# Performance work log

Measured on AMD Instinct MI355X. Metric: run time of the kernel, lower is better.

The kernel has to match this reference:

```python
import jax, jax.numpy as jnp
import numpy as np
from jax import lax

K = 20
SLOPE = 0.01


def setup_inputs() -> dict:
    key = jax.random.key(0)
    k1, k2 = jax.random.split(key)
    x = jax.random.normal(k1, (8, 64, 4096), dtype=jnp.float32)
    # Conv2d(2*64, 64, kernel_size=1, bias=False) weight, squeezed to (out, in)
    W = jax.random.normal(k2, (64, 128), dtype=jnp.float32) * 0.05
    return {"x": x, "W": W}


def reference(x, W):
    # x: (B, C, N), W: (O, 2C)
    B, C, N = x.shape
    # --- knn: pairwise_distance[b,i,j] = -||x_i||^2 + 2 x_i.x_j - ||x_j||^2 ---
    xx = jnp.sum(x * x, axis=1)                      # (B, N)
    inner = jnp.einsum('bcn,bcm->bnm', x, x)         # (B, N, N)
    pdist = 2.0 * inner - xx[:, :, None] - xx[:, None, :]
    idx = lax.top_k(pdist, K)[1]                     # (B, N, K) neighbor indices
    # --- get_graph_feature: gather neighbors, diff + center concat ---
    x_t = jnp.transpose(x, (0, 2, 1))                # (B, N, C)
    neigh = x_t[jnp.arange(B)[:, None, None], idx]   # (B, N, K, C)
    center = x_t[:, :, None, :]                      # (B, N, 1, C)
    feat = jnp.concatenate(
        [neigh - center, jnp.broadcast_to(center, (B, N, K, C))], axis=-1
    )                                                # (B, N, K, 2C)
    # --- 1x1 conv (no bias) + LeakyReLU ---
    h = jnp.einsum('bnkd,od->bonk', feat, W)         # (B, O, N, K)
    h = jnp.where(h >= 0, h, SLOPE * h)
    # --- max over neighbors ---
    return jnp.max(h, axis=-1)                       # (B, O, N)
```

## Files before the change

### kernel.cpp

```cpp
#include <hip/hip_runtime.h>
#include <cfloat>

#define B_ 8
#define C_ 64
#define N_ 4096
#define K_ 20
#define MARGIN 0.08f
#define CAP 64

typedef float f32x4v  __attribute__((ext_vector_type(4)));
typedef float f32x16v __attribute__((ext_vector_type(16)));
typedef _Float16 f16x8 __attribute__((ext_vector_type(8)));
typedef unsigned long long u64;

#define OFF_IDX 131072
#define OFF_QG  2752512
#define OFF_P0  19529728
#define OFF_P1  23724032

__global__ __launch_bounds__(256) void k_split(const float* __restrict__ x,
                                               unsigned short* __restrict__ p0,
                                               unsigned short* __restrict__ p1,
                                               float* __restrict__ xxn) {
    int b = blockIdx.x & 7, mt = blockIdx.x >> 3;
    int m = mt * 256 + threadIdx.x;
    const float* xb = x + (size_t)b * C_ * N_;
    double ss = 0.0;
#pragma unroll 1
    for (int seg = 0; seg < 8; ++seg) {
        unsigned short h0[8], h1[8];
#pragma unroll
        for (int j = 0; j < 8; ++j) {
            float v = xb[(size_t)(seg * 8 + j) * N_ + m];
            ss += (double)v * (double)v;
            _Float16 a = (_Float16)v;
            float r = v - (float)a;
            _Float16 bq = (_Float16)(r * 4096.f);
            h0[j] = __builtin_bit_cast(unsigned short, a);
            h1[j] = __builtin_bit_cast(unsigned short, bq);
        }
        uint4 q0, q1;
        q0.x = h0[0] | (h0[1] << 16); q0.y = h0[2] | (h0[3] << 16);
        q0.z = h0[4] | (h0[5] << 16); q0.w = h0[6] | (h0[7] << 16);
        q1.x = h1[0] | (h1[1] << 16); q1.y = h1[2] | (h1[3] << 16);
        q1.z = h1[4] | (h1[5] << 16); q1.w = h1[6] | (h1[7] << 16);
        size_t o16 = (size_t)(b * 8 + seg) * N_ + m;
        ((uint4*)p0)[o16] = q0;
        ((uint4*)p1)[o16] = q1;
    }
    xxn[b * N_ + m] = (float)(-0.5 * ss);
}

__device__ __forceinline__ void score4(const char* sm, const float* xxs,
                                       int mlb, int mf, int h,
                                       const f16x8 b0[4], float s[16]) {
    f32x16v acc;
#pragma unroll
    for (int g2i = 0; g2i < 4; ++g2i) {
        f32x4v xv = *(const f32x4v*)&xxs[mlb + 4 * h + 8 * g2i];
#pragma unroll
        for (int q = 0; q < 4; ++q) acc[g2i * 4 + q] = xv[q];
    }
#pragma unroll
    for (int kc = 0; kc < 4; ++kc) {
        int seg = kc * 2 + h;
        f16x8 a0 = __builtin_bit_cast(f16x8,
            *(const f32x4v*)(sm + seg * 4096 + (mlb + mf) * 16));
        acc = __builtin_amdgcn_mfma_f32_32x32x16_f16(a0, b0[kc], acc, 0, 0, 0);
    }
#pragma unroll
    for (int r = 0; r < 16; ++r) s[r] = acc[r];
}

__device__ __forceinline__ void score16(const char* sm, const float* xxs,
                                        int mlb, int mf, int h,
                                        const f16x8 b0[4], const f16x8 b1[4],
                                        float s[16]) {
    const float c12 = 1.f / 4096.f;
    f32x16v acc1, acc2, acc3;
#pragma unroll
    for (int g2i = 0; g2i < 4; ++g2i) {
        f32x4v xv = *(const f32x4v*)&xxs[mlb + 4 * h + 8 * g2i];
#pragma unroll
        for (int q = 0; q < 4; ++q) {
            acc1[g2i * 4 + q] = xv[q];
            acc2[g2i * 4 + q] = 0.f;
            acc3[g2i * 4 + q] = 0.f;
        }
    }
#pragma unroll
    for (int kc = 0; kc < 4; ++kc) {
        int seg = kc * 2 + h;
        const char* pA = sm + seg * 4096 + (mlb + mf) * 16;
        f16x8 a0 = __builtin_bit_cast(f16x8, *(const f32x4v*)pA);
        f16x8 a1 = __builtin_bit_cast(f16x8, *(const f32x4v*)(pA + 32768));
        acc1 = __builtin_amdgcn_mfma_f32_32x32x16_f16(a0, b0[kc], acc1, 0, 0, 0);
        acc2 = __builtin_amdgcn_mfma_f32_32x32x16_f16(a0, b1[kc], acc2, 0, 0, 0);
        acc2 = __builtin_amdgcn_mfma_f32_32x32x16_f16(a1, b0[kc], acc2, 0, 0, 0);
        acc3 = __builtin_amdgcn_mfma_f32_32x32x16_f16(a1, b1[kc], acc3, 0, 0, 0);
    }
#pragma unroll
    for (int r = 0; r < 16; ++r)
        s[r] = acc1[r] + (acc2[r] + acc3[r] * c12) * c12;
}

__global__ __launch_bounds__(512, 4) void k_topk(const unsigned short* __restrict__ p0g,
                                                 const unsigned short* __restrict__ p1g,
                                                 const float* __restrict__ xxn,
                                                 u64* __restrict__ bufg,
                                                 int* __restrict__ idxo) {
    __shared__ __align__(16) char smem[67328];
    int b = blockIdx.x & 7, nt = blockIdx.x >> 3;
    int n0 = nt * 64;
    int tid = threadIdx.x;
    int w = tid >> 6, l = tid & 63, h = l >> 5, mf = l & 31;
    int cs = w >> 1, wg = w & 1;
    int rowl = wg * 32 + mf;
    int b8 = b * 8;
    const f32x4v* g0 = (const f32x4v*)p0g;
    const f32x4v* g1 = (const f32x4v*)p1g;
    float* Mp   = (float*)(smem + 32768);
    float* xxs  = (float*)(smem + 65792);
    int*   cntp = (int*)(smem + 66816);
    float* T2p  = (float*)(smem + 67072);

    f16x8 b0[4], b1[4];
#pragma unroll
    for (int kc = 0; kc < 4; ++kc) {
        int seg = kc * 2 + h;
        size_t gi = (size_t)(b8 + seg) * N_ + n0 + rowl;
        b0[kc] = __builtin_bit_cast(f16x8, g0[gi]);
        b1[kc] = __builtin_bit_cast(f16x8, g1[gi]);
    }

#pragma unroll 1
    for (int ch = 0; ch < 16; ++ch) {
        __syncthreads();
#pragma unroll
        for (int i = 0; i < 4; ++i) {
            int lin = i * 512 + tid;
            int seg = lin >> 8, ml = lin & 255;
            *(f32x4v*)(smem + seg * 4096 + ml * 16) =
                g0[(size_t)(b8 + seg) * N_ + ch * 256 + ml];
        }
        if (tid < 256) xxs[tid] = xxn[b * N_ + ch * 256 + tid];
        __syncthreads();
#pragma unroll
        for (int t = 0; t < 2; ++t) {
            int mlb = cs * 64 + t * 32;
            float s[16];
            score4(smem, xxs, mlb, mf, h, b0, s);
            float m8[8];
#pragma unroll
            for (int r = 0; r < 8; ++r) m8[r] = fmaxf(s[r], s[r + 8]);
            float mx = fmaxf(fmaxf(fmaxf(m8[0], m8[1]), fmaxf(m8[2], m8[3])),
                             fmaxf(fmaxf(m8[4], m8[5]), fmaxf(m8[6], m8[7])));
            mx = fmaxf(mx, __shfl_xor(mx, 32));
            if (l < 32)
                Mp[rowl * 129 + ch * 8 + t * 4 + cs] = mx;
        }
    }

    __syncthreads();
    if (tid < 256) {
        int row = tid >> 2, q = tid & 3;
        const float* mrow = Mp + row * 129 + q * 32;
        float v8[8];
#pragma unroll
        for (int j = 0; j < 8; ++j) v8[j] = -FLT_MAX;
#pragma unroll
        for (int i = 0; i < 32; ++i) {
            float v = mrow[i];
#pragma unroll
            for (int j = 7; j >= 1; --j) {
                bool c1 = v > v8[j - 1];
                float nv = c1 ? v8[j - 1] : v;
                v8[j] = (v > v8[j]) ? nv : v8[j];
            }
            v8[0] = fmaxf(v8[0], v);
        }
        float* lp = (float*)smem + row * 33 + q * 8;
#pragma unroll
        for (int j = 0; j < 8; ++j) lp[j] = v8[j];
    }
    __syncthreads();
    if (tid < 64) {
        const float* lp = (const float*)smem + tid * 33;
        float hv0 = lp[0], hv1 = lp[8], hv2 = lp[16], hv3 = lp[24];
        int p0 = 0, p1 = 0, p2 = 0, p3 = 0;
        float tstar = -FLT_MAX;
        for (int k = 0; k < 20; ++k) {
            bool a = hv0 >= hv1; float ma = a ? hv0 : hv1; int sa = a ? 0 : 1;
            bool bb = hv2 >= hv3; float mb = bb ? hv2 : hv3; int sb = bb ? 2 : 3;
            bool c = ma >= mb; tstar = c ? ma : mb; int sl = c ? sa : sb;
            if (sl == 0) { ++p0; hv0 = (p0 < 8) ? lp[p0] : -FLT_MAX; }
            else if (sl == 1) { ++p1; hv1 = (p1 < 8) ? lp[8 + p1] : -FLT_MAX; }
            else if (sl == 2) { ++p2; hv2 = (p2 < 8) ? lp[16 + p2] : -FLT_MAX; }
            else { ++p3; hv3 = (p3 < 8) ? lp[24 + p3] : -FLT_MAX; }
        }
        T2p[tid] = tstar - MARGIN;
        cntp[tid] = 0;
    }
    __syncthreads();
    float T2r = T2p[rowl];

#pragma unroll 1
    for (int ch = 0; ch < 16; ++ch) {
        __syncthreads();
#pragma unroll
        for (int i = 0; i < 8; ++i) {
            int lin = i * 512 + tid;
            int panel = lin >> 11;
            int rem = lin & 2047;
            int seg = rem >> 8, ml = rem & 255;
            size_t gi = (size_t)(b8 + seg) * N_ + ch * 256 + ml;
            const f32x4v* src = panel ? g1 : g0;
            *(f32x4v*)(smem + panel * 32768 + seg * 4096 + ml * 16) = src[gi];
        }
        if (tid < 256) xxs[tid] = xxn[b * N_ + ch * 256 + tid];
        __syncthreads();
#pragma unroll
        for (int t = 0; t < 2; ++t) {
            int mlb = cs * 64 + t * 32;
            float s[16];
            score16(smem, xxs, mlb, mf, h, b0, b1, s);
            unsigned msk = 0;
#pragma unroll
            for (int r = 0; r < 16; ++r) msk |= (s[r] >= T2r) ? (1u << r) : 0u;
            int cb = ch * 256 + mlb + 4 * h;
            while (msk) {
                int r = __ffs(msk) - 1;
                msk &= msk - 1;
                int cand = cb + (r & 3) + 8 * (r >> 2);
                float sv = s[r];
                unsigned sb = __float_as_uint(sv);
                unsigned kk = (sv < 0.f) ? ~sb : (sb | 0x80000000u);
                int slot = atomicAdd(cntp + rowl, 1);
                if (slot < CAP)
                    bufg[((size_t)(b * N_ + n0 + rowl)) * CAP + slot] =
                        ((u64)kk << 32) | (unsigned)(~cand);
            }
        }
    }

    __syncthreads();
    u64* keys = (u64*)smem;
#pragma unroll
    for (int i = 0; i < 8; ++i) {
        int p = i * 512 + tid;
        int row = p >> 6, slot = p & 63;
        int c_ = cntp[row]; c_ = (c_ > CAP) ? CAP : c_;
        u64 key = 0;
        if (slot < c_)
            key = bufg[((size_t)(b * N_ + n0 + row)) * CAP + slot];
        keys[row * (CAP + 1) + slot] = key;
    }
    __syncthreads();
    if (tid < 64) {
        int c_ = cntp[tid]; c_ = (c_ > CAP) ? CAP : c_;
        u64* kp = keys + tid * (CAP + 1);
        int* op = idxo + ((size_t)b * N_ + n0 + tid) * K_;
        for (int k = 0; k < K_; ++k) {
            u64 best = 0; int bs = 0;
            for (int s2 = 0; s2 < c_; ++s2) {
                bool g = kp[s2] > best;
                best = g ? kp[s2] : best;
                bs = g ? s2 : bs;
            }
            op[k] = (int)(~(unsigned)best) & 0xFFF;
            kp[bs] = 0;
        }
    }
}

__global__ __launch_bounds__(256) void k_qg(const float* __restrict__ x,
                                            const float* __restrict__ W,
                                            float* __restrict__ qg) {
    __shared__ float Wl[64 * 129];
    __shared__ float xs[64 * 64];
    int b = blockIdx.x & 7, mt = blockIdx.x >> 3;
    int mbase = mt * 64;
    int tid = threadIdx.x;

    for (int i = 0; i < 32; ++i) {
        int lin = tid + 256 * i;
        int c = lin & 63, o2 = lin >> 6;
        float wv;
        if (o2 < 64) wv = W[o2 * 128 + c];
        else { int o = o2 - 64; wv = W[o * 128 + 64 + c] - W[o * 128 + c]; }
        Wl[c * 129 + o2] = wv;
    }
#pragma unroll
    for (int i = 0; i < 4; ++i) {
        int lin = tid + 256 * i;
        int c = lin >> 4, f = lin & 15;
        *(float4*)&xs[c * 64 + f * 4] =
            *(const float4*)&x[((size_t)b * C_ + c) * N_ + mbase + f * 4];
    }
    __syncthreads();

    int u = tid & 63, half = tid >> 6;
    float a0[16], a1[16];
#pragma unroll
    for (int j = 0; j < 16; ++j) { a0[j] = 0.f; a1[j] = 0.f; }
#pragma unroll 4
    for (int c = 0; c < 64; ++c) {
        float2 wv = *(const float2*)&Wl[c * 129 + 2 * u];
        const float4* xr = (const float4*)&xs[c * 64 + half * 16];
        float4 v0 = xr[0], v1 = xr[1], v2 = xr[2], v3 = xr[3];
        float xvv[16];
        xvv[0]=v0.x; xvv[1]=v0.y; xvv[2]=v0.z; xvv[3]=v0.w;
        xvv[4]=v1.x; xvv[5]=v1.y; xvv[6]=v1.z; xvv[7]=v1.w;
        xvv[8]=v2.x; xvv[9]=v2.y; xvv[10]=v2.z; xvv[11]=v2.w;
        xvv[12]=v3.x; xvv[13]=v3.y; xvv[14]=v3.z; xvv[15]=v3.w;
#pragma unroll
        for (int j = 0; j < 16; ++j) { a0[j] += wv.x * xvv[j]; a1[j] += wv.y * xvv[j]; }
    }
#pragma unroll
    for (int j = 0; j < 16; ++j) {
        int m = mbase + half * 16 + j;
        float2 o; o.x = a0[j]; o.y = a1[j];
        *(float2*)&qg[((size_t)b * N_ + m) * 128 + 2 * u] = o;
    }
}

__global__ __launch_bounds__(256) void k_out(const float* __restrict__ qg,
                                             const int* __restrict__ idxi,
                                             float* __restrict__ out) {
    __shared__ float T[32][65];
    int b = blockIdx.x & 7, nt = blockIdx.x >> 3;
    int n0 = nt * 32;
    int tid = threadIdx.x;
    int w = tid >> 6, o = tid & 63;
    const float* qgb = qg + (size_t)b * N_ * 128;
    for (int i = 0; i < 8; ++i) {
        int nl = w * 8 + i;
        int n = n0 + nl;
        float gv = qgb[(size_t)n * 128 + 64 + o];
        const int* ip = idxi + ((size_t)b * N_ + n) * K_;
        float mx = -FLT_MAX;
#pragma unroll 5
        for (int k = 0; k < K_; ++k) {
            int ik = ip[k];
            float hh = qgb[(size_t)ik * 128 + o] + gv;
            hh = (hh >= 0.f) ? hh : 0.01f * hh;
            mx = fmaxf(mx, hh);
        }
        T[nl][o] = mx;
    }
    __syncthreads();
    int ow = tid >> 2, q = tid & 3;
#pragma unroll
    for (int j4 = 0; j4 < 2; ++j4) {
        int nl = q * 8 + j4 * 4;
        float4 v;
        v.x = T[nl + 0][ow]; v.y = T[nl + 1][ow];
        v.z = T[nl + 2][ow]; v.w = T[nl + 3][ow];
        *(float4*)&out[((size_t)b * 64 + ow) * N_ + n0 + nl] = v;
    }
}

extern "C" void kernel_launch(void* const* d_in, const int* in_sizes, int n_in,
                              void* d_out, int out_size, void* d_ws, size_t ws_size,
                              hipStream_t stream) {
    const float* x = (const float*)d_in[0];
    const float* W = (const float*)d_in[1];
    float* out = (float*)d_out;

    float*          xxn  = (float*)d_ws;
    int*            idx  = (int*)((char*)d_ws + OFF_IDX);
    float*          qg   = (float*)((char*)d_ws + OFF_QG);
    u64*            bufg = (u64*)((char*)d_ws + OFF_QG);
    unsigned short* p0   = (unsigned short*)((char*)d_ws + OFF_P0);
    unsigned short* p1   = (unsigned short*)((char*)d_ws + OFF_P1);

    k_split<<<dim3(128), dim3(256), 0, stream>>>(x, p0, p1, xxn);
    k_topk <<<dim3(512), dim3(512), 0, stream>>>(p0, p1, xxn, bufg, idx);
    k_qg   <<<dim3(512), dim3(256), 0, stream>>>(x, W, qg);
    k_out  <<<dim3(1024), dim3(256), 0, stream>>>(qg, idx, out);
}
```

Measured before the change: 254.5 us.

## Load score operands straight from global memory, dropping LDS staging and barriers

Both scoring passes in k_topk no longer stage 256-column chunks of the fp16 panels into shared memory behind two barriers. Each wave now reads its A fragments and squared norms directly from global memory (L2-cached) over its own 1024-column slice. Shared memory shrinks to hold only the max table, the merge lists and the counters, which may allow more resident blocks. The cost is that each wave issues its own global loads with no cooperative staging, and the chunk-to-wave column mapping changes.

```diff
diff --git a/kernel.cpp b/kernel.cpp
--- a/kernel.cpp
+++ b/kernel.cpp
@@ -51,65 +51,12 @@
     xxn[b * N_ + m] = (float)(-0.5 * ss);
 }
 
-__device__ __forceinline__ void score4(const char* sm, const float* xxs,
-                                       int mlb, int mf, int h,
-                                       const f16x8 b0[4], float s[16]) {
-    f32x16v acc;
-#pragma unroll
-    for (int g2i = 0; g2i < 4; ++g2i) {
-        f32x4v xv = *(const f32x4v*)&xxs[mlb + 4 * h + 8 * g2i];
-#pragma unroll
-        for (int q = 0; q < 4; ++q) acc[g2i * 4 + q] = xv[q];
-    }
-#pragma unroll
-    for (int kc = 0; kc < 4; ++kc) {
-        int seg = kc * 2 + h;
-        f16x8 a0 = __builtin_bit_cast(f16x8,
-            *(const f32x4v*)(sm + seg * 4096 + (mlb + mf) * 16));
-        acc = __builtin_amdgcn_mfma_f32_32x32x16_f16(a0, b0[kc], acc, 0, 0, 0);
-    }
-#pragma unroll
-    for (int r = 0; r < 16; ++r) s[r] = acc[r];
-}
-
-__device__ __forceinline__ void score16(const char* sm, const float* xxs,
-                                        int mlb, int mf, int h,
-                                        const f16x8 b0[4], const f16x8 b1[4],
-                                        float s[16]) {
-    const float c12 = 1.f / 4096.f;
-    f32x16v acc1, acc2, acc3;
-#pragma unroll
-    for (int g2i = 0; g2i < 4; ++g2i) {
-        f32x4v xv = *(const f32x4v*)&xxs[mlb + 4 * h + 8 * g2i];
-#pragma unroll
-        for (int q = 0; q < 4; ++q) {
-            acc1[g2i * 4 + q] = xv[q];
-            acc2[g2i * 4 + q] = 0.f;
-            acc3[g2i * 4 + q] = 0.f;
-        }
-    }
-#pragma unroll
-    for (int kc = 0; kc < 4; ++kc) {
-        int seg = kc * 2 + h;
-        const char* pA = sm + seg * 4096 + (mlb + mf) * 16;
-        f16x8 a0 = __builtin_bit_cast(f16x8, *(const f32x4v*)pA);
-        f16x8 a1 = __builtin_bit_cast(f16x8, *(const f32x4v*)(pA + 32768));
-        acc1 = __builtin_amdgcn_mfma_f32_32x32x16_f16(a0, b0[kc], acc1, 0, 0, 0);
-        acc2 = __builtin_amdgcn_mfma_f32_32x32x16_f16(a0, b1[kc], acc2, 0, 0, 0);
-        acc2 = __builtin_amdgcn_mfma_f32_32x32x16_f16(a1, b0[kc], acc2, 0, 0, 0);
-        acc3 = __builtin_amdgcn_mfma_f32_32x32x16_f16(a1, b1[kc], acc3, 0, 0, 0);
-    }
-#pragma unroll
-    for (int r = 0; r < 16; ++r)
-        s[r] = acc1[r] + (acc2[r] + acc3[r] * c12) * c12;
-}
-
 __global__ __launch_bounds__(512, 4) void k_topk(const unsigned short* __restrict__ p0g,
                                                  const unsigned short* __restrict__ p1g,
                                                  const float* __restrict__ xxn,
                                                  u64* __restrict__ bufg,
                                                  int* __restrict__ idxo) {
-    __shared__ __align__(16) char smem[67328];
+    __shared__ __align__(16) char smem[41984];
     int b = blockIdx.x & 7, nt = blockIdx.x >> 3;
     int n0 = nt * 64;
     int tid = threadIdx.x;
@@ -119,10 +66,12 @@
     int b8 = b * 8;
     const f32x4v* g0 = (const f32x4v*)p0g;
     const f32x4v* g1 = (const f32x4v*)p1g;
-    float* Mp   = (float*)(smem + 32768);
-    float* xxs  = (float*)(smem + 65792);
-    int*   cntp = (int*)(smem + 66816);
-    float* T2p  = (float*)(smem + 67072);
+    const float*  xxb = xxn + b * N_;
+    float* Mp   = (float*)smem;
+    float* Lp   = (float*)(smem + 33024);
+    int*   cntp = (int*)(smem + 41472);
+    float* T2p  = (float*)(smem + 41728);
+    const float c12 = 1.f / 4096.f;
 
     f16x8 b0[4], b1[4];
 #pragma unroll
@@ -133,32 +82,30 @@
         b1[kc] = __builtin_bit_cast(f16x8, g1[gi]);
     }
 
-#pragma unroll 1
-    for (int ch = 0; ch < 16; ++ch) {
-        __syncthreads();
-#pragma unroll
-        for (int i = 0; i < 4; ++i) {
-            int lin = i * 512 + tid;
-            int seg = lin >> 8, ml = lin & 255;
-            *(f32x4v*)(smem + seg * 4096 + ml * 16) =
-                g0[(size_t)(b8 + seg) * N_ + ch * 256 + ml];
-        }
-        if (tid < 256) xxs[tid] = xxn[b * N_ + ch * 256 + tid];
-        __syncthreads();
-#pragma unroll
-        for (int t = 0; t < 2; ++t) {
-            int mlb = cs * 64 + t * 32;
-            float s[16];
-            score4(smem, xxs, mlb, mf, h, b0, s);
-            float m8[8];
-#pragma unroll
-            for (int r = 0; r < 8; ++r) m8[r] = fmaxf(s[r], s[r + 8]);
-            float mx = fmaxf(fmaxf(fmaxf(m8[0], m8[1]), fmaxf(m8[2], m8[3])),
-                             fmaxf(fmaxf(m8[4], m8[5]), fmaxf(m8[6], m8[7])));
-            mx = fmaxf(mx, __shfl_xor(mx, 32));
-            if (l < 32)
-                Mp[rowl * 129 + ch * 8 + t * 4 + cs] = mx;
-        }
+#pragma unroll 2
+    for (int ti = 0; ti < 32; ++ti) {
+        int mc = cs * 1024 + ti * 32;
+        f32x16v acc;
+#pragma unroll
+        for (int g2i = 0; g2i < 4; ++g2i) {
+            f32x4v xv = *(const f32x4v*)&xxb[mc + 4 * h + 8 * g2i];
+#pragma unroll
+            for (int q = 0; q < 4; ++q) acc[g2i * 4 + q] = xv[q];
+        }
+#pragma unroll
+        for (int kc = 0; kc < 4; ++kc) {
+            int seg = kc * 2 + h;
+            f16x8 a0 = __builtin_bit_cast(f16x8, g0[(size_t)(b8 + seg) * N_ + mc + mf]);
+            acc = __builtin_amdgcn_mfma_f32_32x32x16_f16(a0, b0[kc], acc, 0, 0, 0);
+        }
+        float m8[8];
+#pragma unroll
+        for (int r = 0; r < 8; ++r) m8[r] = fmaxf(acc[r], acc[r + 8]);
+        float mx = fmaxf(fmaxf(fmaxf(m8[0], m8[1]), fmaxf(m8[2], m8[3])),
+                         fmaxf(fmaxf(m8[4], m8[5]), fmaxf(m8[6], m8[7])));
+        mx = fmaxf(mx, __shfl_xor(mx, 32));
+        if (l < 32)
+            Mp[rowl * 129 + cs * 32 + ti] = mx;
     }
 
     __syncthreads();
@@ -179,13 +126,13 @@
             }
             v8[0] = fmaxf(v8[0], v);
         }
-        float* lp = (float*)smem + row * 33 + q * 8;
+        float* lp = Lp + row * 33 + q * 8;
 #pragma unroll
         for (int j = 0; j < 8; ++j) lp[j] = v8[j];
     }
     __syncthreads();
     if (tid < 64) {
-        const float* lp = (const float*)smem + tid * 33;
+        const float* lp = Lp + tid * 33;
         float hv0 = lp[0], hv1 = lp[8], hv2 = lp[16], hv3 = lp[24];
         int p0 = 0, p1 = 0, p2 = 0, p3 = 0;
         float tstar = -FLT_MAX;
@@ -205,41 +152,49 @@
     float T2r = T2p[rowl];
 
 #pragma unroll 1
-    for (int ch = 0; ch < 16; ++ch) {
-        __syncthreads();
-#pragma unroll
-        for (int i = 0; i < 8; ++i) {
-            int lin = i * 512 + tid;
-            int panel = lin >> 11;
-            int rem = lin & 2047;
-            int seg = rem >> 8, ml = rem & 255;
-            size_t gi = (size_t)(b8 + seg) * N_ + ch * 256 + ml;
-            const f32x4v* src = panel ? g1 : g0;
-            *(f32x4v*)(smem + panel * 32768 + seg * 4096 + ml * 16) = src[gi];
-        }
-        if (tid < 256) xxs[tid] = xxn[b * N_ + ch * 256 + tid];
-        __syncthreads();
-#pragma unroll
-        for (int t = 0; t < 2; ++t) {
-            int mlb = cs * 64 + t * 32;
-            float s[16];
-            score16(smem, xxs, mlb, mf, h, b0, b1, s);
-            unsigned msk = 0;
-#pragma unroll
-            for (int r = 0; r < 16; ++r) msk |= (s[r] >= T2r) ? (1u << r) : 0u;
-            int cb = ch * 256 + mlb + 4 * h;
-            while (msk) {
-                int r = __ffs(msk) - 1;
-                msk &= msk - 1;
-                int cand = cb + (r & 3) + 8 * (r >> 2);
-                float sv = s[r];
-                unsigned sb = __float_as_uint(sv);
-                unsigned kk = (sv < 0.f) ? ~sb : (sb | 0x80000000u);
-                int slot = atomicAdd(cntp + rowl, 1);
-                if (slot < CAP)
-                    bufg[((size_t)(b * N_ + n0 + rowl)) * CAP + slot] =
-                        ((u64)kk << 32) | (unsigned)(~cand);
+    for (int ti = 0; ti < 32; ++ti) {
+        int mc = cs * 1024 + ti * 32;
+        f32x16v acc1, acc2, acc3;
+#pragma unroll
+        for (int g2i = 0; g2i < 4; ++g2i) {
+            f32x4v xv = *(const f32x4v*)&xxb[mc + 4 * h + 8 * g2i];
+#pragma unroll
+            for (int q = 0; q < 4; ++q) {
+                acc1[g2i * 4 + q] = xv[q];
+                acc2[g2i * 4 + q] = 0.f;
+                acc3[g2i * 4 + q] = 0.f;
             }
+        }
+#pragma unroll
+        for (int kc = 0; kc < 4; ++kc) {
+            int seg = kc * 2 + h;
+            size_t gi = (size_t)(b8 + seg) * N_ + mc + mf;
+            f16x8 a0 = __builtin_bit_cast(f16x8, g0[gi]);
+            f16x8 a1 = __builtin_bit_cast(f16x8, g1[gi]);
+            acc1 = __builtin_amdgcn_mfma_f32_32x32x16_f16(a0, b0[kc], acc1, 0, 0, 0);
+            acc2 = __builtin_amdgcn_mfma_f32_32x32x16_f16(a0, b1[kc], acc2, 0, 0, 0);
+            acc2 = __builtin_amdgcn_mfma_f32_32x32x16_f16(a1, b0[kc], acc2, 0, 0, 0);
+            acc3 = __builtin_amdgcn_mfma_f32_32x32x16_f16(a1, b1[kc], acc3, 0, 0, 0);
+        }
+        float s[16];
+#pragma unroll
+        for (int r = 0; r < 16; ++r)
+            s[r] = acc1[r] + (acc2[r] + acc3[r] * c12) * c12;
+        unsigned msk = 0;
+#pragma unroll
+        for (int r = 0; r < 16; ++r) msk |= (s[r] >= T2r) ? (1u << r) : 0u;
+        int cb = mc + 4 * h;
+        while (msk) {
+            int r = __ffs(msk) - 1;
+            msk &= msk - 1;
+            int cand = cb + (r & 3) + 8 * (r >> 2);
+            float sv = s[r];
+            unsigned sb = __float_as_uint(sv);
+            unsigned kk = (sv < 0.f) ? ~sb : (sb | 0x80000000u);
+            int slot = atomicAdd(cntp + rowl, 1);
+            if (slot < CAP)
+                bufg[((size_t)(b * N_ + n0 + rowl)) * CAP + slot] =
+                    ((u64)kk << 32) | (unsigned)(~cand);
         }
     }
 
```

Measured after the change: 265.6 us. +4.4%, slower.
